# Kernel tuning notes

Measured on AMD Instinct MI355X. Metric: run time of the kernel, lower is better.

## Reference

```python
import jax, jax.numpy as jnp
import numpy as np

B, L, D, H = 4, 256, 256, 8
DH = D // H


def setup_inputs() -> dict:
    key = jax.random.key(0)
    ks = jax.random.split(key, 12)
    s = 1.0 / np.sqrt(D)
    return {
        "inputs": jax.random.normal(ks[0], (B, L, D), jnp.float32),
        "mask": jax.random.bernoulli(ks[1], 0.15, (B, L, L)),
        "rel_emb": jax.random.normal(ks[2], (B, L, L, D), jnp.float32) * 0.05,
        "Wq": jax.random.normal(ks[3], (D, D), jnp.float32) * s,
        "bq": jnp.zeros((D,), jnp.float32),
        "Wk": jax.random.normal(ks[4], (D, D), jnp.float32) * s,
        "bk": jnp.zeros((D,), jnp.float32),
        "Wv": jax.random.normal(ks[5], (D, D), jnp.float32) * s,
        "bv": jnp.zeros((D,), jnp.float32),
        "Wo": jax.random.normal(ks[6], (D, D), jnp.float32) * s,
        "bo": jnp.zeros((D,), jnp.float32),
        "u": jax.random.normal(ks[7], (D,), jnp.float32),
        "v_param": jax.random.normal(ks[8], (D,), jnp.float32),
    }


def _shape(x):
    # (B, L, D) -> (B, H, L, DH)
    return x.reshape(B, L, H, DH).transpose(0, 2, 1, 3)


def reference(inputs, mask, rel_emb, Wq, bq, Wk, bk, Wv, bv, Wo, bo, u, v_param):
    q = _shape(inputs @ Wq.T + bq) / np.sqrt(DH)  # (B,H,L,DH), pre-scaled
    k = _shape(inputs @ Wk.T + bk)
    val = _shape(inputs @ Wv.T + bv)

    u_h = u.reshape(1, H, 1, DH)
    v_h = v_param.reshape(1, H, 1, DH)

    # content term: (q+u) k^T
    a_c = jnp.einsum('bhqd,bhkd->bhqk', q + u_h, k)
    # position term: (q+v) rel_emb^T, rel_emb per (q,k) pair
    rel = rel_emb.reshape(B, L, L, H, DH)
    b_d = jnp.einsum('bhqd,bqkhd->bhqk', q + v_h, rel)

    scores = (a_c + b_d).astype(jnp.float32)
    scores = jnp.where(mask[:, None, :, :], -1e18, scores)
    attn = jax.nn.softmax(scores, axis=-1)  # (B,H,L,L)

    ctx = jnp.einsum('bhqk,bhkd->bhqd', attn, val)
    ctx = ctx.transpose(0, 2, 1, 3).reshape(B, L, D)
    out = ctx @ Wo.T + bo
    return (out, attn)
```

## Files before the change

kernel.cpp:

```cpp
#include <hip/hip_runtime.h>
#include <hip/hip_bf16.h>

#define BB  4
#define LL  256
#define DD  256
#define HH  8
#define DHH 32
#define BL  1024

typedef __attribute__((ext_vector_type(4))) float f32x4;

__global__ __launch_bounds__(256) void qkv_kernel(
    const float* __restrict__ X,
    const float* __restrict__ Wq, const float* __restrict__ bq,
    const float* __restrict__ Wk, const float* __restrict__ bk,
    const float* __restrict__ Wv, const float* __restrict__ bv,
    const float* __restrict__ u,  const float* __restrict__ vp,
    const unsigned int* __restrict__ mask_w,
    float* __restrict__ qu, float* __restrict__ qv,
    float* __restrict__ K,  float* __restrict__ V,
    unsigned int* __restrict__ flags) {
  const int t = threadIdx.x;
  if (blockIdx.x == 256) {
    __shared__ int sf32, shib;
    if (t == 0) { sf32 = 0; shib = 0; }
    __syncthreads();
    int f = 0, hb = 0;
    for (int i = t; i < 16384; i += 256) {
      unsigned int x = mask_w[i];
      if (x == 0x3F800000u) f = 1;
      else if (x & 0xFFFFFF00u) hb = 1;
    }
    if (f)  atomicOr(&sf32, 1);
    if (hb) atomicOr(&shib, 1);
    __syncthreads();
    if (t == 0) flags[0] = (sf32 || !shib) ? 1u : 0u;
    return;
  }
  const int row0 = blockIdx.x * 4;
  const int c = t;
  float accq[4] = {0.f, 0.f, 0.f, 0.f};
  float acck[4] = {0.f, 0.f, 0.f, 0.f};
  float accv[4] = {0.f, 0.f, 0.f, 0.f};
  const float4* Wq4 = (const float4*)(Wq + c * DD);
  const float4* Wk4 = (const float4*)(Wk + c * DD);
  const float4* Wv4 = (const float4*)(Wv + c * DD);
  const float4* X4  = (const float4*)X;
  const int xbase = row0 * (DD / 4);
#pragma unroll 8
  for (int j4 = 0; j4 < DD / 4; ++j4) {
    const float4 wq = Wq4[j4], wk = Wk4[j4], wv = Wv4[j4];
#pragma unroll
    for (int r = 0; r < 4; ++r) {
      const float4 x = X4[xbase + r * (DD / 4) + j4];
      accq[r] += x.x * wq.x + x.y * wq.y + x.z * wq.z + x.w * wq.w;
      acck[r] += x.x * wk.x + x.y * wk.y + x.z * wk.z + x.w * wk.w;
      accv[r] += x.x * wv.x + x.y * wv.y + x.z * wv.z + x.w * wv.w;
    }
  }
  const float scale = 0.17677669529663687f;
  const float uc = u[c], vc = vp[c], bqc = bq[c], bkc = bk[c], bvc = bv[c];
#pragma unroll
  for (int r = 0; r < 4; ++r) {
    const int idx = (row0 + r) * DD + c;
    const float pq = (accq[r] + bqc) * scale;
    qu[idx] = pq + uc;
    qv[idx] = pq + vc;
    K[idx]  = acck[r] + bkc;
    V[idx]  = accv[r] + bvc;
  }
}

__global__ __launch_bounds__(512, 4) void attn_kernel(
    const float* __restrict__ qu, const float* __restrict__ qv,
    const float* __restrict__ Km, const float* __restrict__ Vm,
    const float* __restrict__ rel, const void* __restrict__ mask_raw,
    const unsigned int* __restrict__ flags,
    float* __restrict__ attn_out, float* __restrict__ ctx) {
  const int blk = blockIdx.x;
  const int xcd = blk & 7;
  const int b = xcd >> 1;
  const int q0 = ((xcd & 1) * 64 + (blk >> 3)) * 2;
  const int t = threadIdx.x;
  const int wave = t >> 6, lane = t & 63;
  __shared__ float qu_s[2][DD], qv_s[2][DD];
  __shared__ float msk_s[2][LL];
  __shared__ float sc[2][HH][LL + 4];
  __shared__ float pctx[2][HH][DD + 4];

  {
    const int qq = t >> 8, d = t & 255;
    const int bq = b * LL + q0 + qq;
    qu_s[qq][d] = qu[bq * DD + d];
    qv_s[qq][d] = qv[bq * DD + d];
    bool masked;
    if (flags[0]) masked = ((const unsigned int*)mask_raw)[bq * LL + d] != 0u;
    else          masked = ((const unsigned char*)mask_raw)[bq * LL + d] != 0;
    msk_s[qq][d] = masked ? 1.f : 0.f;
  }
  __syncthreads();

  const float4 u40 = ((const float4*)qu_s[0])[lane];
  const float4 u41 = ((const float4*)qu_s[1])[lane];
  const float4 w40 = ((const float4*)qv_s[0])[lane];
  const float4 w41 = ((const float4*)qv_s[1])[lane];
  const int hol = lane >> 3;
  const int k0 = wave * 32;
  const float4* K4  = (const float4*)(Km + (size_t)b * LL * DD) +
                      (size_t)k0 * 64 + lane;
  const f32x4* R40 = (const f32x4*)rel +
                     (size_t)(b * LL + q0) * (LL * 64) + (size_t)k0 * 64 + lane;
  const f32x4* R41 = R40 + (size_t)LL * 64;
#pragma unroll 4
  for (int i = 0; i < 32; ++i) {
    const int k = k0 + i;
    const float4 kk = K4[(size_t)i * 64];
    const f32x4 r0 = __builtin_nontemporal_load(R40 + (size_t)i * 64);
    const f32x4 r1 = __builtin_nontemporal_load(R41 + (size_t)i * 64);
    float s0 = u40.x * kk.x + u40.y * kk.y + u40.z * kk.z + u40.w * kk.w
             + w40.x * r0.x + w40.y * r0.y + w40.z * r0.z + w40.w * r0.w;
    float s1 = u41.x * kk.x + u41.y * kk.y + u41.z * kk.z + u41.w * kk.w
             + w41.x * r1.x + w41.y * r1.y + w41.z * r1.z + w41.w * r1.w;
    s0 += __shfl_xor(s0, 1); s0 += __shfl_xor(s0, 2); s0 += __shfl_xor(s0, 4);
    s1 += __shfl_xor(s1, 1); s1 += __shfl_xor(s1, 2); s1 += __shfl_xor(s1, 4);
    if ((lane & 7) == 0) {
      sc[0][hol][k] = (msk_s[0][k] != 0.f) ? -1e18f : s0;
      sc[1][hol][k] = (msk_s[1][k] != 0.f) ? -1e18f : s1;
    }
  }
  __syncthreads();

#pragma unroll
  for (int pp = 0; pp < 2; ++pp) {
    const int pair = wave + pp * 8;
    const int qq = pair >> 3, h = pair & 7;
    float v0 = sc[qq][h][lane], v1 = sc[qq][h][lane + 64];
    float v2 = sc[qq][h][lane + 128], v3 = sc[qq][h][lane + 192];
    float m = fmaxf(fmaxf(v0, v1), fmaxf(v2, v3));
#pragma unroll
    for (int off = 32; off >= 1; off >>= 1) m = fmaxf(m, __shfl_xor(m, off));
    float e0 = __expf(v0 - m), e1 = __expf(v1 - m);
    float e2 = __expf(v2 - m), e3 = __expf(v3 - m);
    float s = (e0 + e1) + (e2 + e3);
#pragma unroll
    for (int off = 32; off >= 1; off >>= 1) s += __shfl_xor(s, off);
    const float inv = 1.0f / s;
    e0 *= inv; e1 *= inv; e2 *= inv; e3 *= inv;
    sc[qq][h][lane] = e0; sc[qq][h][lane + 64] = e1;
    sc[qq][h][lane + 128] = e2; sc[qq][h][lane + 192] = e3;
    float* aout = attn_out + (((size_t)(b * HH + h) * LL + (q0 + qq)) * LL);
    __builtin_nontemporal_store(e0, aout + lane);
    __builtin_nontemporal_store(e1, aout + lane + 64);
    __builtin_nontemporal_store(e2, aout + lane + 128);
    __builtin_nontemporal_store(e3, aout + lane + 192);
  }
  __syncthreads();

  {
    const float4* V4 = (const float4*)(Vm + (size_t)b * LL * DD) +
                       (size_t)k0 * 64 + lane;
    float4 a0 = make_float4(0.f, 0.f, 0.f, 0.f);
    float4 a1 = make_float4(0.f, 0.f, 0.f, 0.f);
#pragma unroll 4
    for (int i = 0; i < 32; ++i) {
      const int k = k0 + i;
      const float p0 = sc[0][hol][k];
      const float p1 = sc[1][hol][k];
      const float4 vv = V4[(size_t)i * 64];
      a0.x += p0 * vv.x; a0.y += p0 * vv.y; a0.z += p0 * vv.z; a0.w += p0 * vv.w;
      a1.x += p1 * vv.x; a1.y += p1 * vv.y; a1.z += p1 * vv.z; a1.w += p1 * vv.w;
    }
    ((float4*)&pctx[0][wave][0])[lane] = a0;
    ((float4*)&pctx[1][wave][0])[lane] = a1;
  }
  __syncthreads();

  {
    const int qq = t >> 8, d = t & 255;
    float s = 0.f;
#pragma unroll
    for (int w = 0; w < HH; ++w) s += pctx[qq][w][d];
    ctx[(size_t)(b * LL + q0 + qq) * DD + d] = s;
  }
}

__global__ __launch_bounds__(256) void outproj_kernel(
    const float* __restrict__ ctx, const float* __restrict__ Wo,
    const float* __restrict__ bo, float* __restrict__ out) {
  const int row0 = blockIdx.x * 4;
  const int c = threadIdx.x;
  float acc[4] = {0.f, 0.f, 0.f, 0.f};
  const float4* W4 = (const float4*)(Wo + c * DD);
  const float4* X4 = (const float4*)ctx;
  const int xbase = row0 * (DD / 4);
#pragma unroll 8
  for (int j4 = 0; j4 < DD / 4; ++j4) {
    const float4 w = W4[j4];
#pragma unroll
    for (int r = 0; r < 4; ++r) {
      const float4 x = X4[xbase + r * (DD / 4) + j4];
      acc[r] += x.x * w.x + x.y * w.y + x.z * w.z + x.w * w.w;
    }
  }
  const float boc = bo[c];
#pragma unroll
  for (int r = 0; r < 4; ++r) out[(row0 + r) * DD + c] = acc[r] + boc;
}

extern "C" void kernel_launch(void* const* d_in, const int* in_sizes, int n_in,
                              void* d_out, int out_size, void* d_ws, size_t ws_size,
                              hipStream_t stream) {
  (void)in_sizes; (void)n_in; (void)out_size; (void)ws_size;
  const float* X   = (const float*)d_in[0];
  const void*  msk = d_in[1];
  const float* rel = (const float*)d_in[2];
  const float* Wq  = (const float*)d_in[3];
  const float* bq  = (const float*)d_in[4];
  const float* Wk  = (const float*)d_in[5];
  const float* bk  = (const float*)d_in[6];
  const float* Wv  = (const float*)d_in[7];
  const float* bv  = (const float*)d_in[8];
  const float* Wo  = (const float*)d_in[9];
  const float* bo  = (const float*)d_in[10];
  const float* u   = (const float*)d_in[11];
  const float* vp  = (const float*)d_in[12];

  float* out  = (float*)d_out;
  float* attn = out + BL * DD;

  float* ws_f = (float*)d_ws;
  float* qu  = ws_f;
  float* qv  = qu + BL * DD;
  float* K   = qv + BL * DD;
  float* V   = K  + BL * DD;
  float* ctx = V  + BL * DD;
  unsigned int* flags = (unsigned int*)(ctx + BL * DD);

  qkv_kernel<<<257, 256, 0, stream>>>(X, Wq, bq, Wk, bk, Wv, bv, u, vp,
                                      (const unsigned int*)msk,
                                      qu, qv, K, V, flags);
  attn_kernel<<<BL / 2, 512, 0, stream>>>(qu, qv, K, V, rel, msk, flags,
                                          attn, ctx);
  outproj_kernel<<<BL / 4, 256, 0, stream>>>(ctx, Wo, bo, out);
}
```

Baseline: 97.59 us.

## Fuse output projection into attention kernel and double QKV rows per block

```diff
diff --git a/kernel.cpp b/kernel.cpp
--- a/kernel.cpp
+++ b/kernel.cpp
@@ -21,7 +21,7 @@
     float* __restrict__ K,  float* __restrict__ V,
     unsigned int* __restrict__ flags) {
   const int t = threadIdx.x;
-  if (blockIdx.x == 256) {
+  if (blockIdx.x == 128) {
     __shared__ int sf32, shib;
     if (t == 0) { sf32 = 0; shib = 0; }
     __syncthreads();
@@ -37,21 +37,21 @@
     if (t == 0) flags[0] = (sf32 || !shib) ? 1u : 0u;
     return;
   }
-  const int row0 = blockIdx.x * 4;
+  const int row0 = blockIdx.x * 8;
   const int c = t;
-  float accq[4] = {0.f, 0.f, 0.f, 0.f};
-  float acck[4] = {0.f, 0.f, 0.f, 0.f};
-  float accv[4] = {0.f, 0.f, 0.f, 0.f};
+  float accq[8], acck[8], accv[8];
+#pragma unroll
+  for (int r = 0; r < 8; ++r) { accq[r] = 0.f; acck[r] = 0.f; accv[r] = 0.f; }
   const float4* Wq4 = (const float4*)(Wq + c * DD);
   const float4* Wk4 = (const float4*)(Wk + c * DD);
   const float4* Wv4 = (const float4*)(Wv + c * DD);
   const float4* X4  = (const float4*)X;
   const int xbase = row0 * (DD / 4);
-#pragma unroll 8
+#pragma unroll 4
   for (int j4 = 0; j4 < DD / 4; ++j4) {
     const float4 wq = Wq4[j4], wk = Wk4[j4], wv = Wv4[j4];
 #pragma unroll
-    for (int r = 0; r < 4; ++r) {
+    for (int r = 0; r < 8; ++r) {
       const float4 x = X4[xbase + r * (DD / 4) + j4];
       accq[r] += x.x * wq.x + x.y * wq.y + x.z * wq.z + x.w * wq.w;
       acck[r] += x.x * wk.x + x.y * wk.y + x.z * wk.z + x.w * wk.w;
@@ -61,7 +61,7 @@
   const float scale = 0.17677669529663687f;
   const float uc = u[c], vc = vp[c], bqc = bq[c], bkc = bk[c], bvc = bv[c];
 #pragma unroll
-  for (int r = 0; r < 4; ++r) {
+  for (int r = 0; r < 8; ++r) {
     const int idx = (row0 + r) * DD + c;
     const float pq = (accq[r] + bqc) * scale;
     qu[idx] = pq + uc;
@@ -76,7 +76,8 @@
     const float* __restrict__ Km, const float* __restrict__ Vm,
     const float* __restrict__ rel, const void* __restrict__ mask_raw,
     const unsigned int* __restrict__ flags,
-    float* __restrict__ attn_out, float* __restrict__ ctx) {
+    const float* __restrict__ Wo, const float* __restrict__ bo,
+    float* __restrict__ attn_out, float* __restrict__ out) {
   const int blk = blockIdx.x;
   const int xcd = blk & 7;
   const int b = xcd >> 1;
@@ -87,6 +88,7 @@
   __shared__ float msk_s[2][LL];
   __shared__ float sc[2][HH][LL + 4];
   __shared__ float pctx[2][HH][DD + 4];
+  __shared__ float ctx_s[2][DD];
 
   {
     const int qq = t >> 8, d = t & 255;
@@ -180,31 +182,23 @@
     float s = 0.f;
 #pragma unroll
     for (int w = 0; w < HH; ++w) s += pctx[qq][w][d];
-    ctx[(size_t)(b * LL + q0 + qq) * DD + d] = s;
-  }
-}
-
-__global__ __launch_bounds__(256) void outproj_kernel(
-    const float* __restrict__ ctx, const float* __restrict__ Wo,
-    const float* __restrict__ bo, float* __restrict__ out) {
-  const int row0 = blockIdx.x * 4;
-  const int c = threadIdx.x;
-  float acc[4] = {0.f, 0.f, 0.f, 0.f};
-  const float4* W4 = (const float4*)(Wo + c * DD);
-  const float4* X4 = (const float4*)ctx;
-  const int xbase = row0 * (DD / 4);
+    ctx_s[qq][d] = s;
+  }
+  __syncthreads();
+
+  {
+    const int qq = t >> 8, d = t & 255;
+    const float4* W4 = (const float4*)(Wo + d * DD);
+    const float4* C4 = (const float4*)ctx_s[qq];
+    float acc = 0.f;
 #pragma unroll 8
-  for (int j4 = 0; j4 < DD / 4; ++j4) {
-    const float4 w = W4[j4];
-#pragma unroll
-    for (int r = 0; r < 4; ++r) {
-      const float4 x = X4[xbase + r * (DD / 4) + j4];
-      acc[r] += x.x * w.x + x.y * w.y + x.z * w.z + x.w * w.w;
-    }
-  }
-  const float boc = bo[c];
-#pragma unroll
-  for (int r = 0; r < 4; ++r) out[(row0 + r) * DD + c] = acc[r] + boc;
+    for (int j4 = 0; j4 < DD / 4; ++j4) {
+      const float4 w = W4[j4];
+      const float4 c = C4[j4];
+      acc += c.x * w.x + c.y * w.y + c.z * w.z + c.w * w.w;
+    }
+    out[(size_t)(b * LL + q0 + qq) * DD + d] = acc + bo[d];
+  }
 }
 
 extern "C" void kernel_launch(void* const* d_in, const int* in_sizes, int n_in,
@@ -233,13 +227,11 @@
   float* qv  = qu + BL * DD;
   float* K   = qv + BL * DD;
   float* V   = K  + BL * DD;
-  float* ctx = V  + BL * DD;
-  unsigned int* flags = (unsigned int*)(ctx + BL * DD);
-
-  qkv_kernel<<<257, 256, 0, stream>>>(X, Wq, bq, Wk, bk, Wv, bv, u, vp,
+  unsigned int* flags = (unsigned int*)(V + BL * DD);
+
+  qkv_kernel<<<129, 256, 0, stream>>>(X, Wq, bq, Wk, bk, Wv, bv, u, vp,
                                       (const unsigned int*)msk,
                                       qu, qv, K, V, flags);
   attn_kernel<<<BL / 2, 512, 0, stream>>>(qu, qv, K, V, rel, msk, flags,
-                                          attn, ctx);
-  outproj_kernel<<<BL / 4, 256, 0, stream>>>(ctx, Wo, bo, out);
+                                          Wo, bo, attn, out);
 }
```

Result: slower. 132.5 us (+35.7%).
